# Kernel optimization log

Measured on AMD Instinct MI355X. Metric: run time of the kernel, lower is better.

The kernel has to match this reference:

```python
import jax, jax.numpy as jnp
import numpy as np

B, H, L = 1024, 32, 3
D_S, D_ID = 512, 128
D_STEER = 3 * D_S + D_ID  # 1664
D_HID = 2048
HS, DQ = 16, 64
HDQ = HS * DQ  # 1024


def setup_inputs() -> dict:
    key = jax.random.key(0)
    ks = jax.random.split(key, 18)
    n = lambda k, shape, std: jax.random.normal(k, shape, dtype=jnp.float32) * std
    inp = {
        "x": jax.random.normal(ks[0], (B * H, D_STEER), dtype=jnp.float32),
        "id_in": jax.random.normal(ks[1], (B * H, D_ID), dtype=jnp.float32),
        # per-head content MLP params
        "in_proj_w": n(ks[2], (H, D_STEER, D_S), 0.014),
        "in_proj_b": jnp.zeros((H, D_S), jnp.float32),
        "norm_w": jnp.ones((H, L, D_S), jnp.float32),
        "up_w": n(ks[3], (H, L, D_S, D_HID), 0.014),
        "up_b": jnp.zeros((H, L, D_HID), jnp.float32),
        "down_w": n(ks[4], (H, L, D_HID, D_S), (2.0 / D_HID) ** 0.5),
        "down_b": jnp.zeros((H, L, D_S), jnp.float32),
        # q_proj: Linear(D_steer, 2*HDQ) -> GELU -> Linear(2*HDQ, HDQ)
        "q1_w": n(ks[5], (D_STEER, 2 * HDQ), 0.014),
        "q1_b": jnp.zeros((2 * HDQ,), jnp.float32),
        "q2_w": n(ks[6], (2 * HDQ, HDQ), 0.02),
        "q2_b": jnp.zeros((HDQ,), jnp.float32),
        # k_proj: Linear(D_id, 2*HDQ) -> GELU -> Linear(2*HDQ, HDQ)
        "k1_w": n(ks[7], (D_ID, 2 * HDQ), 0.014),
        "k1_b": jnp.zeros((2 * HDQ,), jnp.float32),
        "k2_w": n(ks[8], (2 * HDQ, HDQ), 0.02),
        "k2_b": jnp.zeros((HDQ,), jnp.float32),
    }
    return inp


def _per_head_mlp(x, in_proj_w, in_proj_b, norm_w, up_w, up_b, down_w, down_b):
    # x: [B*H, D_steer] -> [B*H, D_s]
    bh = x.shape[0]
    b = bh // H
    xh = x.reshape(b, H, D_STEER)
    h = jnp.einsum("bhd,hde->bhe", xh, in_proj_w) + in_proj_b[None]
    for i in range(norm_w.shape[1]):
        rms = jax.lax.rsqrt(jnp.mean(h * h, axis=-1, keepdims=True) + 1e-6)
        xn = h * rms * norm_w[:, i][None]
        hid = jax.nn.gelu(jnp.einsum("bhd,hde->bhe", xn, up_w[:, i]) + up_b[:, i][None], approximate=False)
        h = h + jnp.einsum("bhd,hde->bhe", hid, down_w[:, i]) + down_b[:, i][None]
    return h.reshape(bh, D_S)


def reference(x, id_in, in_proj_w, in_proj_b, norm_w, up_w, up_b, down_w, down_b,
              q1_w, q1_b, q2_w, q2_b, k1_w, k1_b, k2_w, k2_b):
    content = _per_head_mlp(x, in_proj_w, in_proj_b, norm_w, up_w, up_b, down_w, down_b)
    q = jax.nn.gelu(x @ q1_w + q1_b, approximate=False) @ q2_w + q2_b
    k = jax.nn.gelu(id_in @ k1_w + k1_b, approximate=False) @ k2_w + k2_b
    # concat outputs: [B*H, D_s + HDQ + HDQ]
    return jnp.concatenate([content, q, k], axis=-1)
```

## Files before the change

kernel.cpp:

```cpp
#include <hip/hip_runtime.h>
#include <hip/hip_bf16.h>
#include <math.h>

#define HH 32
#define LL 3
#define DS 512
#define DID 128
#define DSTEER 1664
#define DHID 2048
#define HDQ 1024
#define BHROWS 32768

typedef __attribute__((ext_vector_type(8))) short short8;
typedef __attribute__((ext_vector_type(4))) float f32x4;

typedef const __attribute__((address_space(1))) unsigned int* gptr_t;
typedef __attribute__((address_space(3))) unsigned int* lptr_t;

#define BAR() __builtin_amdgcn_s_barrier()
#define SB()  __builtin_amdgcn_sched_barrier(0)
#define VMCNT0() asm volatile("s_waitcnt vmcnt(0)")

__device__ __forceinline__ unsigned short f2bf(float f) {
  union { float f; unsigned int u; } x; x.f = f;
  unsigned int r = (x.u + 0x7FFFu + ((x.u >> 16) & 1u)) >> 16;
  return (unsigned short)r;
}
__device__ __forceinline__ unsigned int pk2(float a, float b) {
  return (unsigned int)f2bf(a) | ((unsigned int)f2bf(b) << 16);
}
__device__ __forceinline__ float gelu_fast(float v) {
  float u = 0.79788456080286536f * v * fmaf(0.044715f * v, v, 1.0f);
  u = fminf(fmaxf(u, -9.0f), 9.0f);
  float t = __builtin_amdgcn_exp2f(-2.8853900817779268f * u);
  float r = __builtin_amdgcn_rcpf(1.0f + t);
  float th = fmaf(-2.0f * t, r, 1.0f);
  return 0.5f * v * (1.0f + th);
}

__global__ void cvt_bf16_kernel(const float4* __restrict__ in, uint2* __restrict__ out, long n4) {
  long i = (long)blockIdx.x * blockDim.x + threadIdx.x;
  long stride = (long)gridDim.x * blockDim.x;
  for (; i < n4; i += stride) {
    float4 v = in[i];
    uint2 o; o.x = pk2(v.x, v.y); o.y = pk2(v.z, v.w);
    out[i] = o;
  }
}

__global__ void cvt_permute_kernel(const float4* __restrict__ in, uint4* __restrict__ out) {
  const int s = blockIdx.x;
  const int b = s >> 5, h = s & 31;
  const long d = (long)h * 1024 + b;
  const float4* src = in + (long)s * (DSTEER / 4);
  uint4* dst = out + d * (DSTEER / 8);
  int t = threadIdx.x;
  if (t < DSTEER / 8) {
    float4 a = src[2 * t], c = src[2 * t + 1];
    uint4 o;
    o.x = pk2(a.x, a.y); o.y = pk2(a.z, a.w);
    o.z = pk2(c.x, c.y); o.w = pk2(c.z, c.w);
    dst[t] = o;
  }
}

__global__ void transpose_cvt_kernel(const float* __restrict__ in, long long in_bstride,
                                     unsigned short* __restrict__ out, long long out_bstride,
                                     int R, int C) {
  __shared__ float t[64][33];
  const int r0 = blockIdx.y * 32;
  const int c0 = blockIdx.x * 64;
  const float* bin = in + (long long)blockIdx.z * in_bstride;
  unsigned short* bout = out + (long long)blockIdx.z * out_bstride;
  const int tid = threadIdx.x;
  const int col = tid & 63, rr = tid >> 6;
  #pragma unroll
  for (int j = 0; j < 8; j++) {
    int r = j * 4 + rr;
    t[col][r] = bin[(size_t)(r0 + r) * C + c0 + col];
  }
  __syncthreads();
  const int rq = (tid & 7) * 4;
  const int cc = tid >> 3;
  #pragma unroll
  for (int j = 0; j < 2; j++) {
    int c = j * 32 + cc;
    float v0 = t[c][rq], v1 = t[c][rq + 1], v2 = t[c][rq + 2], v3 = t[c][rq + 3];
    uint2 o; o.x = pk2(v0, v1); o.y = pk2(v2, v3);
    *(uint2*)&bout[(size_t)(c0 + c) * R + r0 + rq] = o;
  }
}

__global__ void rms_scale_kernel(const float* __restrict__ h,
                                 const float* __restrict__ norm_w,
                                 unsigned short* __restrict__ xn, int layer) {
  int gw = (int)((blockIdx.x * blockDim.x + threadIdx.x) >> 6);
  int lane = threadIdx.x & 63;
  if (gw >= BHROWS) return;
  int head = gw >> 10;
  const float4* hr = (const float4*)(h + (size_t)gw * DS);
  float4 v0 = hr[lane * 2], v1 = hr[lane * 2 + 1];
  float ss = v0.x*v0.x + v0.y*v0.y + v0.z*v0.z + v0.w*v0.w
           + v1.x*v1.x + v1.y*v1.y + v1.z*v1.z + v1.w*v1.w;
  #pragma unroll
  for (int off = 32; off > 0; off >>= 1) ss += __shfl_xor(ss, off, 64);
  float r = rsqrtf(ss * (1.0f / DS) + 1e-6f);
  const float4* nw = (const float4*)(norm_w + ((size_t)head * LL + layer) * DS);
  float4 w0 = nw[lane * 2], w1 = nw[lane * 2 + 1];
  uint4 o;
  o.x = pk2(v0.x * r * w0.x, v0.y * r * w0.y);
  o.y = pk2(v0.z * r * w0.z, v0.w * r * w0.w);
  o.z = pk2(v1.x * r * w1.x, v1.y * r * w1.y);
  o.w = pk2(v1.z * r * w1.z, v1.w * r * w1.w);
  *(uint4*)(xn + (size_t)gw * DS + (size_t)lane * 8) = o;
}

template<int EPI>
__global__ __launch_bounds__(512, 2)
void gemm256_kernel(const unsigned short* __restrict__ A, long long a_hstride, long long a_rstride,
                    const unsigned short* __restrict__ Bt, long long b_hstride,
                    const float* __restrict__ bias, int bias_hstride,
                    const float* __restrict__ resid, long long r_hstride, long long r_rstride,
                    void* __restrict__ Cv, long long c_hstride, long long c_rstride,
                    int gx, int tph, int K) {
  __shared__ unsigned short lds[2 * 2 * 256 * 64];
  const int tid = threadIdx.x;
  const int lane = tid & 63;
  const int wave = tid >> 6;
  const int wr = wave >> 2, wc = wave & 3;
  const int ntot = gridDim.x;
  int id = blockIdx.x;
  { int cpx = ntot >> 3; id = (id & 7) * cpx + (id >> 3); }
  const int head = id / tph;
  const int rem = id % tph;
  const int tn = rem % gx, tm = rem / gx;

  const int l3 = lane >> 3;
  const int gslot = ((lane & 7) ^ l3) * 8;
  const int mbase = wave * 8 + l3;
  const int nbase = (wave >> 2) * 64 + (wave & 3) * 8 + l3;
  const unsigned short* pA = A + (size_t)head * a_hstride
                               + (size_t)(tm * 256 + mbase) * a_rstride + gslot;
  const unsigned short* pB = Bt + (size_t)head * b_hstride
                               + (size_t)(tn * 256 + nbase) * K + gslot;
  const size_t aBlk = (size_t)64 * a_rstride;

  const int physk0 = ((lane >> 4) ^ (lane & 7)) * 8;
  const int physk1 = ((4 + (lane >> 4)) ^ (lane & 7)) * 8;
  const int aRow = wr * 128 + (lane & 15);
  const int bRow = wc * 32 + (lane & 15);

  auto stageA = [&](unsigned short* dstA, int h, size_t kels) {
    #pragma unroll
    for (int i = 0; i < 2; ++i)
      __builtin_amdgcn_global_load_lds(
          (gptr_t)(pA + (size_t)(i * 2 + h) * aBlk + kels),
          (lptr_t)(dstA + ((i * 2 + h) * 64 + wave * 8) * 64), 16, 0, 0);
  };
  auto stageB = [&](unsigned short* dstB, int h, size_t kels) {
    #pragma unroll
    for (int i = 0; i < 2; ++i)
      __builtin_amdgcn_global_load_lds(
          (gptr_t)(pB + (size_t)(i * 128 + h * 32) * K + kels),
          (lptr_t)(dstB + (h * 128 + i * 64 + wave * 8) * 64), 16, 0, 0);
  };

  f32x4 acc[8][4];
  #pragma unroll
  for (int i = 0; i < 8; ++i)
    #pragma unroll
    for (int j = 0; j < 4; ++j) acc[i][j] = (f32x4){0.f, 0.f, 0.f, 0.f};
  short8 a[4][2], b[4][2];

  const int T = K >> 6;
  stageA(lds, 0, 0);
  stageA(lds, 1, 0);
  stageB(lds + 16384, 0, 0);
  stageB(lds + 16384, 1, 0);
  VMCNT0();
  SB();
  BAR();

  for (int t = 0; t < T; ++t) {
    unsigned short* rA = lds + (t & 1) * 32768;
    unsigned short* rB = rA + 16384;
    unsigned short* nA = lds + ((t + 1) & 1) * 32768;
    unsigned short* nB = nA + 16384;
    const size_t k1 = (size_t)(t + 1) * 64;
    const bool m1 = (t + 1 < T);

    #pragma unroll
    for (int j = 0; j < 4; ++j) {
      b[j][0] = *(const short8*)&rB[((j >> 1) * 128 + bRow + (j & 1) * 16) * 64 + physk0];
      b[j][1] = *(const short8*)&rB[((j >> 1) * 128 + bRow + (j & 1) * 16) * 64 + physk1];
    }
    #pragma unroll
    for (int i = 0; i < 4; ++i) {
      a[i][0] = *(const short8*)&rA[(aRow + i * 16) * 64 + physk0];
      a[i][1] = *(const short8*)&rA[(aRow + i * 16) * 64 + physk1];
    }
    if (m1) {
      stageA(nA, 0, k1);
      stageA(nA, 1, k1);
      stageB(nB, 0, k1);
      stageB(nB, 1, k1);
    }
    __builtin_amdgcn_s_setprio(1);
    #pragma unroll
    for (int i = 0; i < 4; ++i)
      #pragma unroll
      for (int j = 0; j < 4; ++j) {
        acc[i][j] = __builtin_amdgcn_mfma_f32_16x16x32_bf16(a[i][0], b[j][0], acc[i][j], 0, 0, 0);
        acc[i][j] = __builtin_amdgcn_mfma_f32_16x16x32_bf16(a[i][1], b[j][1], acc[i][j], 0, 0, 0);
      }
    __builtin_amdgcn_s_setprio(0);
    BAR();

    #pragma unroll
    for (int i = 0; i < 4; ++i) {
      a[i][0] = *(const short8*)&rA[(aRow + (4 + i) * 16) * 64 + physk0];
      a[i][1] = *(const short8*)&rA[(aRow + (4 + i) * 16) * 64 + physk1];
    }
    __builtin_amdgcn_s_setprio(1);
    #pragma unroll
    for (int i = 0; i < 4; ++i)
      #pragma unroll
      for (int j = 0; j < 4; ++j) {
        acc[4 + i][j] = __builtin_amdgcn_mfma_f32_16x16x32_bf16(a[i][0], b[j][0], acc[4 + i][j], 0, 0, 0);
        acc[4 + i][j] = __builtin_amdgcn_mfma_f32_16x16x32_bf16(a[i][1], b[j][1], acc[4 + i][j], 0, 0, 0);
      }
    __builtin_amdgcn_s_setprio(0);
    VMCNT0();
    SB();
    BAR();
  }

  const float* bptr = bias + (size_t)head * bias_hstride;
  #pragma unroll
  for (int i = 0; i < 8; ++i) {
    #pragma unroll
    for (int j = 0; j < 4; ++j) {
      #pragma unroll
      for (int r = 0; r < 4; ++r) {
        int rowt = wr * 128 + i * 16 + (lane >> 4) * 4 + r;
        int colt = wc * 64 + j * 16 + (lane & 15);
        int col = tn * 256 + colt;
        size_t row = (size_t)(tm * 256 + rowt);
        size_t cidx = (size_t)head * c_hstride + row * c_rstride + col;
        float v = acc[i][j][r] + bptr[col];
        if (EPI == 1) {
          ((unsigned short*)Cv)[cidx] = f2bf(gelu_fast(v));
        } else if (EPI == 2) {
          v += resid[(size_t)head * r_hstride + row * r_rstride + col];
          ((float*)Cv)[cidx] = v;
        } else {
          ((float*)Cv)[cidx] = v;
        }
      }
    }
  }
}

extern "C" void kernel_launch(void* const* d_in, const int* in_sizes, int n_in,
                              void* d_out, int out_size, void* d_ws, size_t ws_size,
                              hipStream_t stream) {
  const float* x         = (const float*)d_in[0];
  const float* id_in     = (const float*)d_in[1];
  const float* in_proj_w = (const float*)d_in[2];
  const float* in_proj_b = (const float*)d_in[3];
  const float* norm_w    = (const float*)d_in[4];
  const float* up_w      = (const float*)d_in[5];
  const float* up_b      = (const float*)d_in[6];
  const float* down_w    = (const float*)d_in[7];
  const float* down_b    = (const float*)d_in[8];
  const float* q1_w      = (const float*)d_in[9];
  const float* q1_b      = (const float*)d_in[10];
  const float* q2_w      = (const float*)d_in[11];
  const float* q2_b      = (const float*)d_in[12];
  const float* k1_w      = (const float*)d_in[13];
  const float* k1_b      = (const float*)d_in[14];
  const float* k2_w      = (const float*)d_in[15];
  const float* k2_b      = (const float*)d_in[16];
  float* out = (float*)d_out;

  char* ws = (char*)d_ws;
  unsigned short* x_hm  = (unsigned short*)ws; ws += (size_t)BHROWS * DSTEER * 2;
  unsigned short* id_bf = (unsigned short*)ws; ws += (size_t)BHROWS * DID * 2;
  float*          hbuf  = (float*)ws;          ws += (size_t)BHROWS * DS * 4;
  unsigned short* xn    = (unsigned short*)ws; ws += (size_t)BHROWS * DS * 2;
  unsigned short* hid   = (unsigned short*)ws; ws += (size_t)BHROWS * DHID * 2;
  unsigned short* wbuf  = (unsigned short*)ws; ws += (size_t)HH * DHID * DS * 2;

  cvt_permute_kernel<<<BHROWS, 256, 0, stream>>>((const float4*)x, (uint4*)x_hm);
  cvt_bf16_kernel<<<512, 256, 0, stream>>>((const float4*)id_in, (uint2*)id_bf,
                                           (long)BHROWS * DID / 4);

  transpose_cvt_kernel<<<dim3(2 * HDQ / 64, DSTEER / 32, 1), 256, 0, stream>>>(
      q1_w, 0, wbuf, 0, DSTEER, 2 * HDQ);
  gemm256_kernel<1><<<1024, 512, 0, stream>>>(
      x_hm, (long long)1024 * DSTEER, DSTEER, wbuf, 0, q1_b, 0, nullptr, 0, 0,
      hid, (long long)1024 * 2 * HDQ, 2 * HDQ, 8, 32, DSTEER);
  transpose_cvt_kernel<<<dim3(HDQ / 64, 2 * HDQ / 32, 1), 256, 0, stream>>>(
      q2_w, 0, wbuf, 0, 2 * HDQ, HDQ);
  gemm256_kernel<0><<<512, 512, 0, stream>>>(
      hid, (long long)1024 * 2 * HDQ, 2 * HDQ, wbuf, 0, q2_b, 0, nullptr, 0, 0,
      out + 512, 2560, (long long)32 * 2560, 4, 16, 2 * HDQ);

  transpose_cvt_kernel<<<dim3(2 * HDQ / 64, DID / 32, 1), 256, 0, stream>>>(
      k1_w, 0, wbuf, 0, DID, 2 * HDQ);
  gemm256_kernel<1><<<1024, 512, 0, stream>>>(
      id_bf, 0, DID, wbuf, 0, k1_b, 0, nullptr, 0, 0,
      hid, 0, 2 * HDQ, 8, 1024, DID);
  transpose_cvt_kernel<<<dim3(HDQ / 64, 2 * HDQ / 32, 1), 256, 0, stream>>>(
      k2_w, 0, wbuf, 0, 2 * HDQ, HDQ);
  gemm256_kernel<0><<<512, 512, 0, stream>>>(
      hid, 0, 2 * HDQ, wbuf, 0, k2_b, 0, nullptr, 0, 0,
      out + 1536, 0, 2560, 4, 512, 2 * HDQ);

  transpose_cvt_kernel<<<dim3(DS / 64, DSTEER / 32, HH), 256, 0, stream>>>(
      in_proj_w, (long long)DSTEER * DS, wbuf, (long long)DS * DSTEER, DSTEER, DS);
  gemm256_kernel<0><<<256, 512, 0, stream>>>(
      x_hm, (long long)1024 * DSTEER, DSTEER, wbuf, (long long)DS * DSTEER,
      in_proj_b, DS, nullptr, 0, 0,
      hbuf, (long long)1024 * DS, DS, 2, 8, DSTEER);

  for (int i = 0; i < LL; i++) {
    rms_scale_kernel<<<8192, 256, 0, stream>>>(hbuf, norm_w, xn, i);
    transpose_cvt_kernel<<<dim3(DHID / 64, DS / 32, HH), 256, 0, stream>>>(
        up_w + (size_t)i * DS * DHID, (long long)LL * DS * DHID,
        wbuf, (long long)DHID * DS, DS, DHID);
    gemm256_kernel<1><<<1024, 512, 0, stream>>>(
        xn, (long long)1024 * DS, DS, wbuf, (long long)DHID * DS,
        up_b + (size_t)i * DHID, LL * DHID, nullptr, 0, 0,
        hid, (long long)1024 * DHID, DHID, 8, 32, DS);
    transpose_cvt_kernel<<<dim3(DS / 64, DHID / 32, HH), 256, 0, stream>>>(
        down_w + (size_t)i * DHID * DS, (long long)LL * DHID * DS,
        wbuf, (long long)DS * DHID, DHID, DS);
    if (i < 2) {
      gemm256_kernel<2><<<256, 512, 0, stream>>>(
          hid, (long long)1024 * DHID, DHID, wbuf, (long long)DS * DHID,
          down_b + (size_t)i * DS, LL * DS,
          hbuf, (long long)1024 * DS, DS,
          hbuf, (long long)1024 * DS, DS, 2, 8, DHID);
    } else {
      gemm256_kernel<2><<<256, 512, 0, stream>>>(
          hid, (long long)1024 * DHID, DHID, wbuf, (long long)DS * DHID,
          down_b + (size_t)i * DS, LL * DS,
          hbuf, (long long)1024 * DS, DS,
          out, 2560, (long long)32 * 2560, 2, 8, DHID);
    }
  }
}
```

Before: 1.594 ms.

## Halve GEMM K-step to 32 with smaller LDS double buffer and single-phase loop

The 256x256 bf16 GEMM now stages a K-slice of 32 instead of 64 per iteration, so the double-buffered LDS footprint halves to 64KB. The staging layout, swizzle and per-lane global pointers are reworked to match. Each iteration issues the next stage first, loads all 8 A and 4 B fragments, and runs one MFMA phase with one barrier instead of two half-phases. The smaller LDS footprint may help two blocks fit per CU as the launch bounds intend, but it doubles the number of iterations and barriers per K and gives each barrier less compute to hide load latency behind.

```diff
diff --git a/kernel.cpp b/kernel.cpp
--- a/kernel.cpp
+++ b/kernel.cpp
@@ -123,7 +123,7 @@
                     const float* __restrict__ resid, long long r_hstride, long long r_rstride,
                     void* __restrict__ Cv, long long c_hstride, long long c_rstride,
                     int gx, int tph, int K) {
-  __shared__ unsigned short lds[2 * 2 * 256 * 64];
+  __shared__ unsigned short lds[2 * 2 * 256 * 32];
   const int tid = threadIdx.x;
   const int lane = tid & 63;
   const int wave = tid >> 6;
@@ -135,105 +135,65 @@
   const int rem = id % tph;
   const int tn = rem % gx, tm = rem / gx;
 
-  const int l3 = lane >> 3;
-  const int gslot = ((lane & 7) ^ l3) * 8;
-  const int mbase = wave * 8 + l3;
-  const int nbase = (wave >> 2) * 64 + (wave & 3) * 8 + l3;
-  const unsigned short* pA = A + (size_t)head * a_hstride
-                               + (size_t)(tm * 256 + mbase) * a_rstride + gslot;
-  const unsigned short* pB = Bt + (size_t)head * b_hstride
-                               + (size_t)(tn * 256 + nbase) * K + gslot;
-  const size_t aBlk = (size_t)64 * a_rstride;
-
-  const int physk0 = ((lane >> 4) ^ (lane & 7)) * 8;
-  const int physk1 = ((4 + (lane >> 4)) ^ (lane & 7)) * 8;
+  const int lloc = wave * 16 + (lane >> 2);
+  const int ksw = ((lane & 3) ^ ((lane >> 3) & 3)) * 8;
+  const int wf = (lloc >> 3) & 7;
+  const int g0 = (lloc >> 6) * 128 + (wf >> 2) * 64 + (wf & 3) * 8 + (lloc & 7);
+  const unsigned short* pA0 = A + (size_t)head * a_hstride
+                                + (size_t)(tm * 256 + lloc) * a_rstride + ksw;
+  const unsigned short* pA1 = A + (size_t)head * a_hstride
+                                + (size_t)(tm * 256 + 128 + lloc) * a_rstride + ksw;
+  const unsigned short* pB0 = Bt + (size_t)head * b_hstride
+                                + (size_t)(tn * 256 + g0) * K + ksw;
+  const unsigned short* pB1 = Bt + (size_t)head * b_hstride
+                                + (size_t)(tn * 256 + g0 + 32) * K + ksw;
+  const int ldst0 = (wave * 16) * 32;
+  const int ldst1 = (128 + wave * 16) * 32;
+
+#define STAGE(buf, kb) do { \
+    __builtin_amdgcn_global_load_lds((gptr_t)(pA0 + (kb)), (lptr_t)((buf) + ldst0), 16, 0, 0); \
+    __builtin_amdgcn_global_load_lds((gptr_t)(pA1 + (kb)), (lptr_t)((buf) + ldst1), 16, 0, 0); \
+    __builtin_amdgcn_global_load_lds((gptr_t)(pB0 + (kb)), (lptr_t)((buf) + 8192 + ldst0), 16, 0, 0); \
+    __builtin_amdgcn_global_load_lds((gptr_t)(pB1 + (kb)), (lptr_t)((buf) + 8192 + ldst1), 16, 0, 0); \
+  } while (0)
+
+  const int physk = ((lane >> 4) ^ ((lane >> 1) & 3)) * 8;
   const int aRow = wr * 128 + (lane & 15);
   const int bRow = wc * 32 + (lane & 15);
 
-  auto stageA = [&](unsigned short* dstA, int h, size_t kels) {
-    #pragma unroll
-    for (int i = 0; i < 2; ++i)
-      __builtin_amdgcn_global_load_lds(
-          (gptr_t)(pA + (size_t)(i * 2 + h) * aBlk + kels),
-          (lptr_t)(dstA + ((i * 2 + h) * 64 + wave * 8) * 64), 16, 0, 0);
-  };
-  auto stageB = [&](unsigned short* dstB, int h, size_t kels) {
-    #pragma unroll
-    for (int i = 0; i < 2; ++i)
-      __builtin_amdgcn_global_load_lds(
-          (gptr_t)(pB + (size_t)(i * 128 + h * 32) * K + kels),
-          (lptr_t)(dstB + (h * 128 + i * 64 + wave * 8) * 64), 16, 0, 0);
-  };
-
   f32x4 acc[8][4];
   #pragma unroll
   for (int i = 0; i < 8; ++i)
     #pragma unroll
     for (int j = 0; j < 4; ++j) acc[i][j] = (f32x4){0.f, 0.f, 0.f, 0.f};
-  short8 a[4][2], b[4][2];
-
-  const int T = K >> 6;
-  stageA(lds, 0, 0);
-  stageA(lds, 1, 0);
-  stageB(lds + 16384, 0, 0);
-  stageB(lds + 16384, 1, 0);
-  VMCNT0();
-  SB();
+
+  const int T = K >> 5;
+  STAGE(lds, 0);
+  VMCNT0(); SB();
   BAR();
 
   for (int t = 0; t < T; ++t) {
-    unsigned short* rA = lds + (t & 1) * 32768;
-    unsigned short* rB = rA + 16384;
-    unsigned short* nA = lds + ((t + 1) & 1) * 32768;
-    unsigned short* nB = nA + 16384;
-    const size_t k1 = (size_t)(t + 1) * 64;
-    const bool m1 = (t + 1 < T);
-
-    #pragma unroll
-    for (int j = 0; j < 4; ++j) {
-      b[j][0] = *(const short8*)&rB[((j >> 1) * 128 + bRow + (j & 1) * 16) * 64 + physk0];
-      b[j][1] = *(const short8*)&rB[((j >> 1) * 128 + bRow + (j & 1) * 16) * 64 + physk1];
-    }
-    #pragma unroll
-    for (int i = 0; i < 4; ++i) {
-      a[i][0] = *(const short8*)&rA[(aRow + i * 16) * 64 + physk0];
-      a[i][1] = *(const short8*)&rA[(aRow + i * 16) * 64 + physk1];
-    }
-    if (m1) {
-      stageA(nA, 0, k1);
-      stageA(nA, 1, k1);
-      stageB(nB, 0, k1);
-      stageB(nB, 1, k1);
-    }
+    unsigned short* cur = lds + (t & 1) * 16384;
+    unsigned short* nxt = lds + ((t + 1) & 1) * 16384;
+    if (t + 1 < T) STAGE(nxt, (size_t)(t + 1) * 32);
+    short8 bfr[4], a[8];
+    #pragma unroll
+    for (int j = 0; j < 4; ++j)
+      bfr[j] = *(const short8*)&cur[8192 + ((j >> 1) * 128 + bRow + (j & 1) * 16) * 32 + physk];
+    #pragma unroll
+    for (int i = 0; i < 8; ++i)
+      a[i] = *(const short8*)&cur[(aRow + i * 16) * 32 + physk];
     __builtin_amdgcn_s_setprio(1);
     #pragma unroll
-    for (int i = 0; i < 4; ++i)
+    for (int i = 0; i < 8; ++i)
       #pragma unroll
-      for (int j = 0; j < 4; ++j) {
-        acc[i][j] = __builtin_amdgcn_mfma_f32_16x16x32_bf16(a[i][0], b[j][0], acc[i][j], 0, 0, 0);
-        acc[i][j] = __builtin_amdgcn_mfma_f32_16x16x32_bf16(a[i][1], b[j][1], acc[i][j], 0, 0, 0);
-      }
+      for (int j = 0; j < 4; ++j)
+        acc[i][j] = __builtin_amdgcn_mfma_f32_16x16x32_bf16(a[i], bfr[j], acc[i][j], 0, 0, 0);
     __builtin_amdgcn_s_setprio(0);
+    VMCNT0(); SB();
     BAR();
-
-    #pragma unroll
-    for (int i = 0; i < 4; ++i) {
-      a[i][0] = *(const short8*)&rA[(aRow + (4 + i) * 16) * 64 + physk0];
-      a[i][1] = *(const short8*)&rA[(aRow + (4 + i) * 16) * 64 + physk1];
-    }
-    __builtin_amdgcn_s_setprio(1);
-    #pragma unroll
-    for (int i = 0; i < 4; ++i)
-      #pragma unroll
-      for (int j = 0; j < 4; ++j) {
-        acc[4 + i][j] = __builtin_amdgcn_mfma_f32_16x16x32_bf16(a[i][0], b[j][0], acc[4 + i][j], 0, 0, 0);
-        acc[4 + i][j] = __builtin_amdgcn_mfma_f32_16x16x32_bf16(a[i][1], b[j][1], acc[4 + i][j], 0, 0, 0);
-      }
-    __builtin_amdgcn_s_setprio(0);
-    VMCNT0();
-    SB();
-    BAR();
-  }
+  }
+#undef STAGE
 
   const float* bptr = bias + (size_t)head * bias_hstride;
   #pragma unroll
```

New measurement: 1.690 ms. 6.0% more time.
